# Optimization experiments

Hardware: AMD Instinct MI355X
Metric: run time of the kernel (lower is better)

Reference implementation:

```python
import jax, jax.numpy as jnp
import numpy as np

EPS = 1e-5
SLOPE = 0.2

def _lrelu(x):
    return jnp.where(x >= 0, x, SLOPE * x)

def _bn(x, axes):
    # BatchNorm in training mode with gamma=1, beta=0 (module defaults), biased var
    m = jnp.mean(x, axis=axes, keepdims=True)
    v = jnp.var(x, axis=axes, keepdims=True)
    return (x - m) * jax.lax.rsqrt(v + EPS)

def _knn(x, k):
    # x: [B, C, N] -> idx [B, N, k] of nearest neighbors (incl. self)
    inner = -2.0 * jnp.einsum('bcn,bcm->bnm', x, x)
    xx = jnp.sum(x * x, axis=1)  # [B, N]
    d = -xx[:, :, None] - inner - xx[:, None, :]  # negative squared dist
    return jax.lax.top_k(d, k)[1]

def _graph_feature(x, k):
    # x: [B, C, N] -> [B, 2C, N, k] of (neighbor - center, center)
    idx = _knn(x, k)                       # [B, N, k]
    xt = jnp.transpose(x, (0, 2, 1))       # [B, N, C]
    feat = jax.vmap(lambda xb, ib: xb[ib])(xt, idx)  # [B, N, k, C]
    center = xt[:, :, None, :]
    out = jnp.concatenate([feat - center, jnp.broadcast_to(center, feat.shape)], axis=-1)
    return jnp.transpose(out, (0, 3, 1, 2))

def _conv2(w, x):   # 1x1 conv2d: x [B,C,N,K]
    return jnp.einsum('oc,bcnk->bonk', w, x)

def _conv1(w, x):   # 1x1 conv1d: x [B,C,N]
    return jnp.einsum('oc,bcn->bon', w, x)

def _pool(xyz, feature, wp, bp, kp):
    # dropout is identity in eval mode
    proj = _conv1(wp, feature) + bp[None, :, None]     # [B, C, N]
    vector = jnp.max(proj, axis=-1, keepdims=True)     # [B, C, 1]
    scores = jax.nn.sigmoid(jnp.sum(feature * vector, axis=1))  # [B, N]
    values, idx = jax.lax.top_k(scores, kp)            # [B, kp]
    node_static = jnp.take_along_axis(xyz, idx[:, None, :], axis=2)
    node_feature = jnp.take_along_axis(feature, idx[:, None, :], axis=2)
    v = values[:, None, :]
    return node_static * v, node_feature * v


def setup_inputs() -> dict:
    key = jax.random.key(0)
    ks = jax.random.split(key, 20)
    def rn(i, shape, s=0.05):
        return jax.random.normal(ks[i], shape, dtype=jnp.float32) * s
    return {
        'x': jax.random.normal(ks[0], (16, 3, 2048), dtype=jnp.float32),
        'w1': rn(1, (64, 6)), 'w2': rn(2, (64, 128)), 'w2m': rn(3, (1024, 128)),
        'w3': rn(4, (128, 256)), 'w4': rn(5, (128, 256)), 'w4m': rn(6, (1024, 256)),
        'w5': rn(7, (256, 512)), 'w5m': rn(8, (1024, 256)),
        'wp1': rn(9, (128, 128)), 'bp1': rn(10, (128,)),
        'wp2': rn(11, (256, 256)), 'bp2': rn(12, (256,)),
        'wl1': rn(13, (512, 3072)),
        'wl2': rn(14, (256, 512)), 'bl2': rn(15, (256,)),
        'wl3': rn(16, (40, 256)), 'bl3': rn(17, (40,)),
    }


def reference(x, w1, w2, w2m, w3, w4, w4m, w5, w5m, wp1, bp1, wp2, bp2, wl1, wl2, bl2, wl3, bl3):
    k = 20
    xyz = x
    # stage 1 (N=2048)
    h = _lrelu(_bn(_conv2(w1, _graph_feature(x, k)), (0, 2, 3)))
    x1 = jnp.max(h, axis=-1)                       # [B, 64, N]
    h = _lrelu(_bn(_conv2(w2, _graph_feature(x1, k)), (0, 2, 3)))
    x2 = jnp.max(h, axis=-1)                       # [B, 64, N]
    xt1_ = jnp.concatenate([x1, x2], axis=1)       # [B, 128, N]
    xt1 = _lrelu(_bn(_conv1(w2m, xt1_), (0, 2)))   # [B, 1024, N]
    node1, nf1 = _pool(xyz, xt1_, wp1, bp1, 256)   # [B,3,256], [B,128,256]
    # stage 2 (256 nodes, k//2)
    h = _lrelu(_bn(_conv2(w3, _graph_feature(nf1, k // 2)), (0, 2, 3)))
    x3 = jnp.max(h, axis=-1)                       # [B, 128, 256]
    h = _lrelu(_bn(_conv2(w4, _graph_feature(x3, k // 2)), (0, 2, 3)))
    x4 = jnp.max(h, axis=-1)
    xt2_ = jnp.concatenate([x3, x4], axis=1)       # [B, 256, 256]
    xt2 = _lrelu(_bn(_conv1(w4m, xt2_), (0, 2)))   # [B, 1024, 256]
    node2, nf2 = _pool(node1, xt2_, wp2, bp2, 64)  # [B,3,64], [B,256,64]
    # stage 3 (64 nodes, k//4)
    h = _lrelu(_bn(_conv2(w5, _graph_feature(nf2, k // 4)), (0, 2, 3)))
    x5 = jnp.max(h, axis=-1)                       # [B, 256, 64]
    xt3 = _lrelu(_bn(_conv1(w5m, x5), (0, 2)))     # [B, 1024, 64]
    # global max pools + head (dropout = identity in eval)
    g = jnp.concatenate([jnp.max(xt1, -1), jnp.max(xt2, -1), jnp.max(xt3, -1)], axis=1)  # [B, 3072]
    h = _lrelu(_bn(g @ wl1.T, (0,)))
    h = _lrelu(_bn(h @ wl2.T + bl2, (0,)))
    out = h @ wl3.T + bl3                          # [B, 40]
    return (out, node1, node2)
```

## Files before the change

kernel.cpp:

```cpp
#include <hip/hip_runtime.h>
#include <cmath>
#include <cstdint>
#include <cstddef>

typedef unsigned int u32;
typedef unsigned short u16;
typedef unsigned long long u64;
typedef __attribute__((ext_vector_type(8))) short short8v;
typedef __attribute__((ext_vector_type(4))) float f32x4;

#define TPB 256
#define EPSV 1e-5f
#define SLP 0.2f

__device__ __forceinline__ float lrelu(float x){ return x >= 0.f ? x : SLP*x; }
__device__ __forceinline__ u32 encf(float f){ u32 u=__float_as_uint(f); return (u&0x80000000u)? ~u : (u|0x80000000u); }
__device__ __forceinline__ float decf(u32 e){ return (e&0x80000000u)? __uint_as_float(e&0x7FFFFFFFu) : __uint_as_float(~e); }
__device__ __forceinline__ u16 f2b(float f){ u32 u=__float_as_uint(f); return (u16)((u + 0x7FFFu + ((u>>16)&1u))>>16); }
__device__ __forceinline__ float b2f(u16 h){ return __uint_as_float(((u32)h)<<16); }

__global__ void k_detect(const u16* __restrict__ raw, int n, int* __restrict__ flag){
  __shared__ float red[TPB];
  int tid=threadIdx.x; float m=0.f;
  for(int i=tid;i<n;i+=TPB){
    float v=fabsf(b2f(raw[i]));
    if(!isnan(v) && !isinf(v) && v>m) m=v;
  }
  red[tid]=m; __syncthreads();
  for(int s=TPB/2;s>0;s>>=1){ if(tid<s) red[tid]=fmaxf(red[tid],red[tid+s]); __syncthreads(); }
  if(tid==0) *flag = (red[0] > 1000.f) ? 1 : 0;
}

struct CvtArgs{ const void* s[18]; float* d[18]; int n[18]; };
__global__ void k_cvt_all(CvtArgs a, const int* __restrict__ flag){
  int z=blockIdx.y; int n=a.n[z]; int f=*flag;
  const void* s=a.s[z]; float* d=a.d[z];
  for(int i=blockIdx.x*TPB+threadIdx.x; i<n; i+=gridDim.x*TPB)
    d[i] = f ? ((const float*)s)[i] : b2f(((const u16*)s)[i]);
}

__global__ void k_castw(const float* __restrict__ W, u16* __restrict__ Wb, int n){
  int i=blockIdx.x*TPB+threadIdx.x; if(i<n) Wb[i]=f2b(W[i]);
}

__global__ void k_xpose_bf(const float* __restrict__ X, u16* __restrict__ Xb,
                           int ldC, int C, int N){
  __shared__ float t[32][33];
  int b=blockIdx.z;
  int c0=blockIdx.y*32, n0=blockIdx.x*32;
  int tx=threadIdx.x&31, ty=threadIdx.x>>5;
  const float* Xs = X + (size_t)b*ldC*N;
  #pragma unroll
  for(int i=0;i<4;i++){
    int c=c0+ty+i*8;
    t[ty+i*8][tx] = (c<C && n0+tx<N) ? Xs[(size_t)c*N + n0+tx] : 0.f;
  }
  __syncthreads();
  u16* Ob = Xb + (size_t)b*N*C;
  #pragma unroll
  for(int i=0;i<4;i++){
    int n=n0+ty+i*8;
    if(n<N && c0+tx<C) Ob[(size_t)n*C + c0+tx] = f2b(t[tx][ty+i*8]);
  }
}

template<int KSTEPS>
__global__ __launch_bounds__(256) void k_convmax_mfma(
    const u16* __restrict__ Wb, const u16* __restrict__ Xb,
    u32* __restrict__ gmaxEnc, int gstride, int g_off, double* __restrict__ stats,
    int C, int N, int O){
  int tid=threadIdx.x, lane=tid&63, w=tid>>6;
  int b=blockIdx.z;
  int oW = blockIdx.y*64 + w*16;
  int nB = blockIdx.x*256;
  int row16 = lane&15, grp = lane>>4;
  short8v af[KSTEPS];
  const u16* Wrow = Wb + (size_t)(oW + row16)*C + grp*8;
  #pragma unroll
  for(int ks=0;ks<KSTEPS;ks++) af[ks] = *(const short8v*)(Wrow + ks*32);
  const short8v zb = {0,0,0,0,0,0,0,0};
  f32x4 acc[16];
  #pragma unroll
  for(int t=0;t<16;t++){
    int n = nB + t*16 + row16;
    bool nv = (n < N);
    const u16* Xrow = Xb + ((size_t)b*N + (nv? n:0))*C + grp*8;
    short8v bf[KSTEPS];
    #pragma unroll
    for(int ks=0;ks<KSTEPS;ks++) bf[ks] = nv ? *(const short8v*)(Xrow + ks*32) : zb;
    f32x4 a = {0.f,0.f,0.f,0.f};
    #pragma unroll
    for(int ks=0;ks<KSTEPS;ks++)
      a = __builtin_amdgcn_mfma_f32_16x16x32_bf16(af[ks], bf[ks], a, 0, 0, 0);
    acc[t]=a;
  }
  float mxr[4], s1r[4], s2r[4];
  #pragma unroll
  for(int r=0;r<4;r++){ mxr[r]=-INFINITY; s1r[r]=0.f; s2r[r]=0.f; }
  #pragma unroll
  for(int t=0;t<16;t++){
    int n = nB + t*16 + row16;
    bool nv = (n<N);
    #pragma unroll
    for(int r=0;r<4;r++){
      float y = acc[t][r];
      if(nv){ mxr[r]=fmaxf(mxr[r],y); s1r[r]+=y; s2r[r]+=y*y; }
    }
  }
  #pragma unroll
  for(int s=1;s<16;s<<=1){
    #pragma unroll
    for(int r=0;r<4;r++){
      mxr[r]=fmaxf(mxr[r], __shfl_xor(mxr[r], s));
      s1r[r]+=__shfl_xor(s1r[r], s);
      s2r[r]+=__shfl_xor(s2r[r], s);
    }
  }
  if(row16==0){
    #pragma unroll
    for(int r=0;r<4;r++){
      int o = oW + grp*4 + r;
      atomicMax(&gmaxEnc[(size_t)b*gstride + g_off + o], encf(mxr[r]));
      atomicAdd(&stats[2*o], (double)s1r[r]);
      atomicAdd(&stats[2*o+1], (double)s2r[r]);
    }
  }
}

__global__ void k_sqnorm(const float* __restrict__ X, float* __restrict__ xx, int B, int ldC, int C, int N){
  int i=blockIdx.x*TPB+threadIdx.x; if(i>=B*N) return;
  int b=i/N, n=i-b*N;
  const float* p = X + ((size_t)b*ldC)*N + n;
  float s=0.f;
  for(int c=0;c<C;c++){ float x=p[(size_t)c*N]; s+=x*x; }
  xx[i]=s;
}

template<int JMAX, int CT>
__global__ __launch_bounds__(256) void k_knn_fused(
    const float* __restrict__ X, const float* __restrict__ xx,
    int ldC, int KSEL, int* __restrict__ idxOut){
  const int N = JMAX*64;
  extern __shared__ float sm[];
  __shared__ u64 cand[4][128];
  int tid=threadIdx.x, lane=tid&63, w=tid>>6;
  int b, row0;
  if constexpr (JMAX==32){
    int lin=blockIdx.x, xcd=lin&7, j=lin>>3;
    b = xcd + ((j>>9)<<3);
    row0 = (j&511)*4;
  } else {
    b = blockIdx.y; row0 = blockIdx.x*4;
  }
  const float* Xb = X + (size_t)b*ldC*N;
  const float* xxb = xx + (size_t)b*N;

  if constexpr (JMAX==32){
    int c0 = tid*4;
    float4 acc0[4], acc1[4];
    #pragma unroll
    for(int r=0;r<4;r++){ acc0[r]=make_float4(0,0,0,0); acc1[r]=make_float4(0,0,0,0); }
    #pragma unroll 4
    for(int c=0;c<CT;c++){
      const float* Xc = Xb + (size_t)c*N;
      float4 b0 = *(const float4*)&Xc[c0];
      float4 b1 = *(const float4*)&Xc[c0+1024];
      #pragma unroll
      for(int r=0;r<4;r++){
        float a = Xc[row0+r];
        acc0[r].x += a*b0.x; acc0[r].y += a*b0.y; acc0[r].z += a*b0.z; acc0[r].w += a*b0.w;
        acc1[r].x += a*b1.x; acc1[r].y += a*b1.y; acc1[r].z += a*b1.z; acc1[r].w += a*b1.w;
      }
    }
    float4 xm0 = *(const float4*)&xxb[c0];
    float4 xm1 = *(const float4*)&xxb[c0+1024];
    #pragma unroll
    for(int r=0;r<4;r++){
      float xr = xxb[row0+r];
      float4 d0, d1;
      d0.x=2.f*acc0[r].x-xr-xm0.x; d0.y=2.f*acc0[r].y-xr-xm0.y;
      d0.z=2.f*acc0[r].z-xr-xm0.z; d0.w=2.f*acc0[r].w-xr-xm0.w;
      d1.x=2.f*acc1[r].x-xr-xm1.x; d1.y=2.f*acc1[r].y-xr-xm1.y;
      d1.z=2.f*acc1[r].z-xr-xm1.z; d1.w=2.f*acc1[r].w-xr-xm1.w;
      *(float4*)&sm[r*N + c0]        = d0;
      *(float4*)&sm[r*N + c0 + 1024] = d1;
    }
  } else {
    int tcol = (tid < N)? tid : (tid & (N-1));
    float acc[4];
    #pragma unroll
    for(int r=0;r<4;r++) acc[r]=0.f;
    #pragma unroll 4
    for(int c=0;c<CT;c++){
      const float* Xc = Xb + (size_t)c*N;
      float bv = Xc[tcol];
      #pragma unroll
      for(int r=0;r<4;r++) acc[r] += Xc[row0+r]*bv;
    }
    float xm = xxb[tcol];
    #pragma unroll
    for(int r=0;r<4;r++) sm[r*N + tcol] = 2.f*acc[r] - xxb[row0+r] - xm;
  }
  __syncthreads();

  u64* cw = cand[w];
  int r = w;
  const float* Sr = sm + (size_t)r*N;
  u32 ev[JMAX];
  if constexpr (JMAX>=4){
    #pragma unroll
    for(int ch=0;ch<JMAX/4;ch++){
      float4 v = *(const float4*)&Sr[ch*256 + lane*4];
      ev[ch*4+0]=encf(v.x); ev[ch*4+1]=encf(v.y); ev[ch*4+2]=encf(v.z); ev[ch*4+3]=encf(v.w);
    }
  } else {
    ev[0]=encf(Sr[lane]);
  }
  int* op = idxOut + ((size_t)b*N + row0 + r)*KSEL;
  if constexpr (JMAX>=8){
    u32 vmax=ev[0];
    #pragma unroll
    for(int j=1;j<JMAX;j++) vmax = vmax>ev[j]? vmax:ev[j];
    u32 lo=0u, hi=0xFFFFFFFFu;
    while(lo<hi){
      u32 d=hi-lo; u32 mid=lo+(d>>1)+(d&1u);
      int cnum=(int)__popcll(__ballot(vmax>=mid));
      if(cnum>=KSEL) lo=mid; else hi=mid-1u;
    }
    u32 T=lo;
    u64 lml=((u64)1<<lane)-1ull;
    u32 base=0;
    #pragma unroll
    for(int j=0;j<JMAX;j++){
      bool p = ev[j]>=T;
      u64 mk=__ballot(p);
      u32 pos=base+(u32)__popcll(mk&lml);
      int m = (j>>2)*256 + lane*4 + (j&3);
      if(p && pos<128u) cw[pos] = ((u64)ev[j]<<32) | (u64)(u32)(~(u32)m);
      base += (u32)__popcll(mk);
    }
    int nc=(int)base;
    if(nc<=64){
      u64 cv = cw[lane];
      if(lane>=nc) cv=0ull;
      #pragma unroll
      for(int kk=2;kk<=64;kk<<=1){
        #pragma unroll
        for(int jj=kk>>1;jj>0;jj>>=1){
          u64 p=__shfl_xor(cv,jj);
          bool takeMax=(((lane&jj)!=0)==((lane&kk)==0));
          u64 mx=cv>p?cv:p, mn=cv>p?p:cv;
          cv=takeMax?mx:mn;
        }
      }
      if(lane>=64-KSEL) op[63-lane]=(int)(~(u32)cv);
    } else if(nc<=128){
      u64 c0v=cw[lane], c1v=cw[64+lane];
      if(64+lane>=nc) c1v=0ull;
      u64 kl=~0ull;
      for(int t=0;t<KSEL;t++){
        u64 bk=(c0v<kl)?c0v:0ull;
        if(c1v<kl&&c1v>bk) bk=c1v;
        #pragma unroll
        for(int s=1;s<64;s<<=1){u64 ok=__shfl_xor(bk,s); if(ok>bk)bk=ok;}
        if(lane==0) op[t]=(int)(~(u32)bk);
        kl=bk;
      }
    } else {
      u64 kl=~0ull;
      for(int t=0;t<KSEL;t++){
        u64 bk=0ull;
        #pragma unroll
        for(int j=0;j<JMAX;j++){
          int m = (j>>2)*256 + lane*4 + (j&3);
          u64 kj=((u64)ev[j]<<32)|(u64)(u32)(~(u32)m);
          if(kj<kl&&kj>bk) bk=kj;
        }
        #pragma unroll
        for(int s=1;s<64;s<<=1){u64 ok=__shfl_xor(bk,s); if(ok>bk)bk=ok;}
        if(lane==0) op[t]=(int)(~(u32)bk);
        kl=bk;
      }
    }
  } else {
    u64 key[JMAX];
    #pragma unroll
    for(int j=0;j<JMAX;j++){
      int m = (JMAX>=4)? ((j>>2)*256 + lane*4 + (j&3)) : lane;
      key[j]=((u64)ev[j]<<32)|(u64)(u32)(~(u32)m);
    }
    u64 kl=~0ull;
    for(int t=0;t<KSEL;t++){
      u64 bk=0ull;
      #pragma unroll
      for(int j=0;j<JMAX;j++){ u64 kj=key[j]; if(kj<kl&&kj>bk) bk=kj; }
      #pragma unroll
      for(int s=1;s<64;s<<=1){u64 ok=__shfl_xor(bk,s); if(ok>bk)bk=ok;}
      if(lane==0) op[t]=(int)(~(u32)bk);
      kl=bk;
    }
  }
}

__global__ void k_topk_sort(const float* __restrict__ S, int M, int K,
                            int* __restrict__ idxOut, float* __restrict__ valOut){
  extern __shared__ u64 key[];
  int b=blockIdx.x, tid=threadIdx.x;
  const float* Sr = S + (size_t)b*M;
  for(int i=tid;i<M;i+=TPB)
    key[i] = ((u64)(~encf(Sr[i]))<<32) | (u32)i;
  __syncthreads();
  for(int k=2;k<=M;k<<=1){
    for(int j=k>>1;j>0;j>>=1){
      for(int i=tid;i<M;i+=TPB){
        int ixj=i^j;
        if(ixj>i){
          u64 a=key[i], c=key[ixj];
          bool up=((i&k)==0);
          if(up ? (a>c) : (a<c)){ key[i]=c; key[ixj]=a; }
        }
      }
      __syncthreads();
    }
  }
  for(int p=tid;p<K;p+=TPB){
    u64 kk=key[p];
    idxOut[(size_t)b*K+p]=(int)(u32)(kk&0xFFFFFFFFull);
    valOut[(size_t)b*K+p]=decf(~(u32)(kk>>32));
  }
}

__global__ __launch_bounds__(256) void k_uv_t(
    const float* __restrict__ X, int ldC, const float* __restrict__ W,
    float* __restrict__ U, float* __restrict__ V, int C, int N, int O){
  extern __shared__ float wsm[];
  int tid=threadIdx.x, b=blockIdx.z;
  int o0=blockIdx.y*8;
  for(int i=tid;i<8*C;i+=TPB){
    int o=i/C, c=i-o*C;
    const float* Wr = W + (size_t)(o0+o)*2*C;
    float wa=Wr[c], wb=Wr[C+c];
    wsm[(size_t)(o*C+c)*2  ]=wa;
    wsm[(size_t)(o*C+c)*2+1]=wb-wa;
  }
  __syncthreads();
  int n=blockIdx.x*TPB+tid;
  bool act=(n<N); int nc=act? n:0;
  const float* Xb = X + ((size_t)b*ldC)*N + nc;
  float u[8], v[8];
  #pragma unroll
  for(int o=0;o<8;o++){ u[o]=0.f; v[o]=0.f; }
  for(int c=0;c<C;c++){
    float x = Xb[(size_t)c*N];
    #pragma unroll
    for(int o=0;o<8;o++){
      float2 wv = *(const float2*)&wsm[(size_t)(o*C+c)*2];
      u[o] += wv.x*x;
      v[o] += wv.y*x;
    }
  }
  if(act){
    #pragma unroll
    for(int o=0;o<8;o++){
      size_t off=((size_t)b*O+o0+o)*N+n;
      U[off]=u[o]; V[off]=v[o];
    }
  }
}

template<int KT, int OT>
__global__ void k_nbr_t(const float* __restrict__ U, const float* __restrict__ V, const int* __restrict__ idx,
                        float* __restrict__ outBase, int ldCout, int ch_off,
                        double* __restrict__ stats, int O, int N){
  __shared__ double redS[4][OT], redQ[4][OT];
  int tid=threadIdx.x, lane=tid&63, wv=tid>>6;
  int n = blockIdx.x*TPB+tid;
  int o0 = blockIdx.y*OT, b = blockIdx.z;
  bool act = (n<N);
  int nc = act? n : (N-1);
  int jr[KT];
  const int* jp = idx + ((size_t)b*N+nc)*KT;
  #pragma unroll
  for(int k=0;k<KT;k++){ int j=jp[k]; jr[k] = ((unsigned)j<(unsigned)N)? j : 0; }
  for(int oo=0;oo<OT;oo++){
    const float* Ur = U + ((size_t)b*O+o0+oo)*N;
    float mx=-INFINITY, s1=0.f, s2=0.f;
    #pragma unroll
    for(int k=0;k<KT;k++){ float u=Ur[jr[k]]; mx=fmaxf(mx,u); s1+=u; s2+=u*u; }
    float v = V[((size_t)b*O+o0+oo)*N+nc];
    if(act) outBase[((size_t)b*ldCout+ch_off+o0+oo)*N+n] = mx+v;
    double cs = act ? ((double)s1 + (double)KT*(double)v) : 0.0;
    double cq = act ? ((double)s2 + 2.0*(double)v*(double)s1 + (double)KT*(double)v*(double)v) : 0.0;
    #pragma unroll
    for(int s=1;s<64;s<<=1){ cs += __shfl_xor(cs,s); cq += __shfl_xor(cq,s); }
    if(lane==0){ redS[wv][oo]=cs; redQ[wv][oo]=cq; }
  }
  __syncthreads();
  if(tid<OT){
    double s=0,q=0;
    #pragma unroll
    for(int w=0;w<4;w++){ s+=redS[w][tid]; q+=redQ[w][tid]; }
    atomicAdd(&stats[2*(o0+tid)], s);
    atomicAdd(&stats[2*(o0+tid)+1], q);
  }
}

__global__ void k_bnact(float* __restrict__ out, int ldCout, int ch_off, const double* __restrict__ stats,
                        int O, int N, double cnt){
  int n=blockIdx.x*TPB+threadIdx.x; if(n>=N) return;
  int o=blockIdx.y, b=blockIdx.z;
  double m=stats[2*o]/cnt;
  double var=stats[2*o+1]/cnt - m*m;
  float s=rsqrtf((float)var+EPSV);
  size_t p=((size_t)b*ldCout+ch_off+o)*N+n;
  float h=out[p];
  out[p] = lrelu((float)((double)h-m)*s);
}

template<int PTS>
__global__ void k_convmax(const float* __restrict__ X, int ldC, const float* __restrict__ W, const float* __restrict__ bias,
                          u32* __restrict__ gmaxEnc, int gstride, int g_off, double* __restrict__ stats,
                          int C, int N, int O){
  __shared__ float red[4*16*3];
  int tid=threadIdx.x, ot=blockIdx.y, b=blockIdx.z;
  int lane=tid&63, wv=tid>>6;
  int n0 = blockIdx.x*TPB*PTS + tid*PTS;
  bool act = (n0 < N);
  int n0c = act ? n0 : (N-PTS);
  const float* Xb = X + ((size_t)b*ldC)*N;
  const float* Wr = W + (size_t)ot*16*C;
  float acc[16][PTS];
  #pragma unroll
  for(int oo=0;oo<16;oo++)
    #pragma unroll
    for(int p=0;p<PTS;p++) acc[oo][p]=0.f;
  for(int c=0;c<C;c+=4){
    float xv[4][PTS];
    #pragma unroll
    for(int cc=0;cc<4;cc++){
      if(PTS==4){
        float4 t = *(const float4*)&Xb[(size_t)(c+cc)*N + n0c];
        xv[cc][0]=t.x; xv[cc][1]=t.y; xv[cc][2]=t.z; xv[cc][3]=t.w;
      } else {
        xv[cc][0]=Xb[(size_t)(c+cc)*N + n0c];
      }
    }
    #pragma unroll
    for(int oo=0;oo<16;oo++){
      float w0=Wr[oo*C+c], w1=Wr[oo*C+c+1], w2=Wr[oo*C+c+2], w3=Wr[oo*C+c+3];
      #pragma unroll
      for(int p=0;p<PTS;p++)
        acc[oo][p] += w0*xv[0][p] + w1*xv[1][p] + w2*xv[2][p] + w3*xv[3][p];
    }
  }
  bool hs = (stats!=nullptr);
  #pragma unroll
  for(int oo=0;oo<16;oo++){
    float bval = bias? bias[ot*16+oo] : 0.f;
    float mx=-INFINITY, s1=0.f, s2=0.f;
    #pragma unroll
    for(int p=0;p<PTS;p++){
      float y=acc[oo][p]+bval;
      if(act && n0+p<N){ mx=fmaxf(mx,y); s1+=y; s2+=y*y; }
    }
    #pragma unroll
    for(int s=1;s<64;s<<=1){
      mx=fmaxf(mx,__shfl_xor(mx,s));
      if(hs){ s1+=__shfl_xor(s1,s); s2+=__shfl_xor(s2,s); }
    }
    if(lane==0){ red[(wv*16+oo)*3]=mx; red[(wv*16+oo)*3+1]=s1; red[(wv*16+oo)*3+2]=s2; }
  }
  __syncthreads();
  if(tid<16){
    int oo=tid, o=ot*16+oo;
    float mx=red[oo*3], s1=red[oo*3+1], s2=red[oo*3+2];
    #pragma unroll
    for(int w=1;w<4;w++){ mx=fmaxf(mx,red[(w*16+oo)*3]); s1+=red[(w*16+oo)*3+1]; s2+=red[(w*16+oo)*3+2]; }
    atomicMax(&gmaxEnc[(size_t)b*gstride+g_off+o], encf(mx));
    if(hs){ atomicAdd(&stats[2*o],(double)s1); atomicAdd(&stats[2*o+1],(double)s2); }
  }
}

__global__ void k_gfinal(const u32* __restrict__ gmaxEnc, int gstride, int g_off, const double* __restrict__ stats,
                         float* __restrict__ G, int B, int O, double cnt){
  int i=blockIdx.x*TPB+threadIdx.x; if(i>=B*O) return;
  int b=i/O, o=i-b*O;
  double m=stats[2*o]/cnt;
  double var=stats[2*o+1]/cnt - m*m;
  float s=rsqrtf((float)var+EPSV);
  float x=decf(gmaxEnc[(size_t)b*gstride+g_off+o]);
  G[(size_t)b*gstride+g_off+o]=lrelu((float)((double)x-m)*s);
}

__global__ void k_scores(const float* __restrict__ X, int ldC, const u32* __restrict__ vecEnc,
                         float* __restrict__ sc, int C, int N){
  int n=blockIdx.x*TPB+threadIdx.x; if(n>=N) return;
  int b=blockIdx.y;
  const float* Xb = X + ((size_t)b*ldC)*N + n;
  double s=0;
  for(int c=0;c<C;c++) s += (double)Xb[(size_t)c*N]*(double)decf(vecEnc[(size_t)b*C+c]);
  float sf=(float)s;
  sc[(size_t)b*N+n]=1.f/(1.f+expf(-sf));
}

__global__ void k_pgather(const float* __restrict__ xyz, int ldCx, const float* __restrict__ feat, int ldCf,
                          const int* __restrict__ pidx, const float* __restrict__ pval,
                          float* __restrict__ nodeOut, float* __restrict__ nfOut, int Cf, int Nin, int Kp){
  int b=blockIdx.y;
  int i=blockIdx.x*TPB+threadIdx.x;
  int total=(3+Cf)*Kp; if(i>=total) return;
  int c=i/Kp, p=i-c*Kp;
  int j=pidx[(size_t)b*Kp+p]; if((unsigned)j>=(unsigned)Nin) j=0;
  float v=pval[(size_t)b*Kp+p];
  if(c<3) nodeOut[((size_t)b*3+c)*Kp+p]=xyz[((size_t)b*ldCx+c)*Nin+j]*v;
  else { int cf=c-3; nfOut[((size_t)b*Cf+cf)*Kp+p]=feat[((size_t)b*ldCf+cf)*Nin+j]*v; }
}

__global__ void k_fc_wave(const float* __restrict__ A, const float* __restrict__ W, const float* __restrict__ bias,
                          float* __restrict__ Y, int B, int IN, int OUT){
  int gw = (blockIdx.x*blockDim.x + threadIdx.x) >> 6;
  if(gw >= B*OUT) return;
  int lane = threadIdx.x & 63;
  int b = gw/OUT, j = gw - b*OUT;
  const float4* a4 = (const float4*)(A + (size_t)b*IN);
  const float4* w4 = (const float4*)(W + (size_t)j*IN);
  int n4 = IN >> 2;
  float s = 0.f;
  for(int t=lane; t<n4; t+=64){
    float4 av=a4[t], wv=w4[t];
    s += av.x*wv.x + av.y*wv.y + av.z*wv.z + av.w*wv.w;
  }
  #pragma unroll
  for(int sh=1; sh<64; sh<<=1) s += __shfl_xor(s, sh);
  if(lane==0) Y[gw] = s + (bias? bias[j]:0.f);
}

__global__ void k_bnb(const float* __restrict__ Y, float* __restrict__ H, int B, int F){
  int f=blockIdx.x*TPB+threadIdx.x; if(f>=F) return;
  double s=0,q=0;
  for(int b=0;b<B;b++){ double y=Y[(size_t)b*F+f]; s+=y; q+=y*y; }
  double m=s/B, var=q/B-m*m;
  float sc=rsqrtf((float)var+EPSV);
  for(int b=0;b<B;b++){ float y=Y[(size_t)b*F+f]; H[(size_t)b*F+f]=lrelu((float)((double)y-m)*sc); }
}

__global__ void k_out(const float* __restrict__ OUTF, const float* __restrict__ N1v, const float* __restrict__ N2v,
                      void* __restrict__ dout, const int* __restrict__ flag){
  int i=blockIdx.x*TPB+threadIdx.x; if(i>=16000) return;
  float v = (i<640)? OUTF[i] : (i<12928)? N1v[i-640] : N2v[i-12928];
  if(*flag) ((float*)dout)[i]=v; else ((u16*)dout)[i]=f2b(v);
}

extern "C" void kernel_launch(void* const* d_in, const int* in_sizes, int n_in,
                              void* d_out, int out_size, void* d_ws, size_t ws_size,
                              hipStream_t stream){
  const int B=16;
  char* basep=(char*)d_ws; size_t off=0;
  auto alloc=[&](size_t elems, size_t esz)->void*{
    off=(off+255)&~(size_t)255; void* p=basep+off; off+=elems*esz; return p;
  };
  const int NINP=18;
  const int insz[NINP]={98304,384,8192,131072,32768,32768,262144,131072,262144,16384,128,65536,256,1572864,131072,256,10240,40};
  float* F[NINP];
  for(int i=0;i<NINP;i++) F[i]=(float*)alloc((size_t)insz[i],4);
  float* XF=F[0];
  float *W1F=F[1],*W2F=F[2],*W2MF=F[3],*W3F=F[4],*W4F=F[5],*W4MF=F[6],*W5F=F[7],*W5MF=F[8],
        *WP1F=F[9],*BP1F=F[10],*WP2F=F[11],*BP2F=F[12],*WL1F=F[13],*WL2F=F[14],*BL2F=F[15],*WL3F=F[16],*BL3F=F[17];
  float* XX  =(float*)alloc((size_t)16*2048,4);
  float* U   =(float*)alloc((size_t)16*64*2048,4);
  float* V   =(float*)alloc((size_t)16*64*2048,4);
  float* XT1 =(float*)alloc((size_t)16*128*2048,4);
  float* XT2 =(float*)alloc((size_t)16*256*256,4);
  float* NF1 =(float*)alloc((size_t)16*128*256,4);
  float* NF2 =(float*)alloc((size_t)16*256*64,4);
  float* X5  =(float*)alloc((size_t)16*256*64,4);
  float* NODE1=(float*)alloc((size_t)16*3*256,4);
  float* NODE2=(float*)alloc((size_t)16*3*64,4);
  float* SCORES=(float*)alloc((size_t)16*2048,4);
  float* PVAL1=(float*)alloc((size_t)16*256,4);
  float* PVAL2=(float*)alloc((size_t)16*64,4);
  float* G   =(float*)alloc((size_t)16*3072,4);
  float* Y1  =(float*)alloc((size_t)16*512,4);
  float* H1  =(float*)alloc((size_t)16*512,4);
  float* Y2  =(float*)alloc((size_t)16*256,4);
  float* H2  =(float*)alloc((size_t)16*256,4);
  float* OUTF=(float*)alloc((size_t)16*40,4);
  u32* GMAX  =(u32*)alloc((size_t)16*3072,4);
  u32* VECENC=(u32*)alloc((size_t)16*256,4);
  int* IDX   =(int*)alloc((size_t)16*2048*20,4);
  int* PIDX1 =(int*)alloc((size_t)16*256,4);
  int* PIDX2 =(int*)alloc((size_t)16*64,4);
  double* STATS=(double*)alloc((size_t)2*1024,8);
  int* FLAG  =(int*)alloc(64,4);
  u16* XTB  =(u16*)alloc((size_t)16*2048*128,2);
  u16* WB2M =(u16*)alloc((size_t)131072,2);
  u16* WB4M =(u16*)alloc((size_t)262144,2);
  u16* WB5M =(u16*)alloc((size_t)262144,2);

  k_detect<<<dim3(1),dim3(TPB),0,stream>>>((const u16*)d_in[1], insz[1], FLAG);
  CvtArgs ca;
  for(int i=0;i<NINP;i++){ ca.s[i]=d_in[i]; ca.d[i]=F[i]; ca.n[i]=insz[i]; }
  k_cvt_all<<<dim3(64,NINP),dim3(TPB),0,stream>>>(ca, FLAG);
  k_castw<<<dim3((131072+TPB-1)/TPB),dim3(TPB),0,stream>>>(W2MF,WB2M,131072);
  k_castw<<<dim3((262144+TPB-1)/TPB),dim3(TPB),0,stream>>>(W4MF,WB4M,262144);
  k_castw<<<dim3((262144+TPB-1)/TPB),dim3(TPB),0,stream>>>(W5MF,WB5M,262144);

  auto knn=[&](const float* X, int ldC, int C, int N, int K){
    k_sqnorm<<<dim3((B*N+TPB-1)/TPB),dim3(TPB),0,stream>>>(X,XX,B,ldC,C,N);
    size_t shm=(size_t)4*N*4;
    if(N==2048 && C==3)       k_knn_fused<32,3>  <<<dim3(8192),dim3(256),shm,stream>>>(X,XX,ldC,K,IDX);
    else if(N==2048)          k_knn_fused<32,64> <<<dim3(8192),dim3(256),shm,stream>>>(X,XX,ldC,K,IDX);
    else if(N==256)           k_knn_fused<4,128> <<<dim3(N/4,B),dim3(256),shm,stream>>>(X,XX,ldC,K,IDX);
    else                      k_knn_fused<1,256> <<<dim3(N/4,B),dim3(256),shm,stream>>>(X,XX,ldC,K,IDX);
  };

  auto graph_conv=[&](const float* X, int ldC, int C, int N, int K, const float* W, int O,
                      float* outBase, int ldCout, int ch_off){
    knn(X,ldC,C,N,K);
    size_t wshm=(size_t)8*C*2*4;
    k_uv_t<<<dim3((N+TPB-1)/TPB,O/8,B),dim3(TPB),wshm,stream>>>(X,ldC,W,U,V,C,N,O);
    hipMemsetAsync(STATS,0,2*(size_t)O*sizeof(double),stream);
    dim3 g((N+TPB-1)/TPB, O/8, B);
    if(K==20)      k_nbr_t<20,8><<<g,dim3(TPB),0,stream>>>(U,V,IDX,outBase,ldCout,ch_off,STATS,O,N);
    else if(K==10) k_nbr_t<10,8><<<g,dim3(TPB),0,stream>>>(U,V,IDX,outBase,ldCout,ch_off,STATS,O,N);
    else           k_nbr_t<5,8> <<<g,dim3(TPB),0,stream>>>(U,V,IDX,outBase,ldCout,ch_off,STATS,O,N);
    double cnt=(double)B*(double)N*(double)K;
    k_bnact<<<dim3((N+TPB-1)/TPB,O,B),dim3(TPB),0,stream>>>(outBase,ldCout,ch_off,STATS,O,N,cnt);
  };

  auto convmax_f32=[&](const float* X,int ldC,const float* W,const float* bias,
                   u32* gmax,int gstride,int g_off,double* stats,int C,int N,int O){
    if(N>=1024) k_convmax<4><<<dim3((N+TPB*4-1)/(TPB*4),O/16,B),dim3(TPB),0,stream>>>(X,ldC,W,bias,gmax,gstride,g_off,stats,C,N,O);
    else        k_convmax<1><<<dim3((N+TPB-1)/TPB,O/16,B),dim3(TPB),0,stream>>>(X,ldC,W,bias,gmax,gstride,g_off,stats,C,N,O);
  };

  auto pool=[&](const float* xyzF,int ldCx,const float* featF,int ldCf,int Cf,int Nin,
                const float* WP,const float* BP,int Op,int Kp,
                float* nodeOut,float* nfOut,int* pidx,float* pval){
    hipMemsetAsync(VECENC,0,(size_t)B*Op*4,stream);
    convmax_f32(featF,ldCf,WP,BP,VECENC,Op,0,(double*)nullptr,Cf,Nin,Op);
    k_scores<<<dim3((Nin+TPB-1)/TPB,B),dim3(TPB),0,stream>>>(featF,ldCf,VECENC,SCORES,Cf,Nin);
    k_topk_sort<<<dim3(B),dim3(TPB),(size_t)Nin*8,stream>>>(SCORES,Nin,Kp,pidx,pval);
    k_pgather<<<dim3(((3+Cf)*Kp+TPB-1)/TPB,B),dim3(TPB),0,stream>>>(xyzF,ldCx,featF,ldCf,pidx,pval,nodeOut,nfOut,Cf,Nin,Kp);
  };

  auto gseg=[&](const float* X,int ldC,int C,int N,const u16* WBc,int g_off,double cnt){
    hipMemsetAsync(STATS,0,2*1024*sizeof(double),stream);
    k_xpose_bf<<<dim3((N+31)/32,(C+31)/32,B),dim3(256),0,stream>>>(X,XTB,ldC,C,N);
    dim3 g((N+255)/256, 1024/64, B);
    if(C==128) k_convmax_mfma<4><<<g,dim3(256),0,stream>>>(WBc,XTB,GMAX,3072,g_off,STATS,C,N,1024);
    else       k_convmax_mfma<8><<<g,dim3(256),0,stream>>>(WBc,XTB,GMAX,3072,g_off,STATS,C,N,1024);
    k_gfinal<<<dim3((B*1024+TPB-1)/TPB),dim3(TPB),0,stream>>>(GMAX,3072,g_off,STATS,G,B,1024,cnt);
  };

  graph_conv(XF,3,3,2048,20,W1F,64,XT1,128,0);
  graph_conv(XT1,128,64,2048,20,W2F,64,XT1,128,64);
  hipMemsetAsync(GMAX,0,(size_t)16*3072*4,stream);
  gseg(XT1,128,128,2048,WB2M,0,(double)16*2048);
  pool(XF,3,XT1,128,128,2048,WP1F,BP1F,128,256,NODE1,NF1,PIDX1,PVAL1);
  graph_conv(NF1,128,128,256,10,W3F,128,XT2,256,0);
  graph_conv(XT2,256,128,256,10,W4F,128,XT2,256,128);
  gseg(XT2,256,256,256,WB4M,1024,(double)16*256);
  pool(NODE1,3,XT2,256,256,256,WP2F,BP2F,256,64,NODE2,NF2,PIDX2,PVAL2);
  graph_conv(NF2,256,256,64,5,W5F,256,X5,256,0);
  gseg(X5,256,256,64,WB5M,2048,(double)16*64);
  k_fc_wave<<<dim3((16*512*64+TPB-1)/TPB),dim3(TPB),0,stream>>>(G,WL1F,(const float*)nullptr,Y1,16,3072,512);
  k_bnb<<<dim3((512+TPB-1)/TPB),dim3(TPB),0,stream>>>(Y1,H1,16,512);
  k_fc_wave<<<dim3((16*256*64+TPB-1)/TPB),dim3(TPB),0,stream>>>(H1,WL2F,BL2F,Y2,16,512,256);
  k_bnb<<<dim3((256+TPB-1)/TPB),dim3(TPB),0,stream>>>(Y2,H2,16,256);
  k_fc_wave<<<dim3((16*40*64+TPB-1)/TPB),dim3(TPB),0,stream>>>(H2,WL3F,BL3F,OUTF,16,256,40);
  k_out<<<dim3((16000+TPB-1)/TPB),dim3(TPB),0,stream>>>(OUTF,NODE1,NODE2,(u16*)d_out,FLAG);
}
```

Baseline: 1.137 ms.

## Split N=2048 kNN distance tile into halves to halve shared memory and registers

For the N=2048 kNN kernel, the distance row block is now computed in two 1024-column halves. Each half reuses a 16 KB shared buffer, and its encoded values are read into registers before the next half is written. This halves dynamic shared memory, drops the second accumulator set, and adds a launch-bounds occupancy hint of 6 blocks. The cost is an extra barrier and reading the X rows twice.

```diff
diff --git a/kernel.cpp b/kernel.cpp
--- a/kernel.cpp
+++ b/kernel.cpp
@@ -137,7 +137,7 @@
 }
 
 template<int JMAX, int CT>
-__global__ __launch_bounds__(256) void k_knn_fused(
+__global__ __launch_bounds__(256, 6) void k_knn_fused(
     const float* __restrict__ X, const float* __restrict__ xx,
     int ldC, int KSEL, int* __restrict__ idxOut){
   const int N = JMAX*64;
@@ -155,35 +155,44 @@
   const float* Xb = X + (size_t)b*ldC*N;
   const float* xxb = xx + (size_t)b*N;
 
+  u32 ev[JMAX];
+
   if constexpr (JMAX==32){
     int c0 = tid*4;
-    float4 acc0[4], acc1[4];
-    #pragma unroll
-    for(int r=0;r<4;r++){ acc0[r]=make_float4(0,0,0,0); acc1[r]=make_float4(0,0,0,0); }
-    #pragma unroll 4
-    for(int c=0;c<CT;c++){
-      const float* Xc = Xb + (size_t)c*N;
-      float4 b0 = *(const float4*)&Xc[c0];
-      float4 b1 = *(const float4*)&Xc[c0+1024];
+    #pragma unroll
+    for(int h=0;h<2;h++){
+      float4 acc0[4];
+      #pragma unroll
+      for(int r=0;r<4;r++) acc0[r]=make_float4(0,0,0,0);
+      #pragma unroll 4
+      for(int c=0;c<CT;c++){
+        const float* Xc = Xb + (size_t)c*N;
+        float4 b0 = *(const float4*)&Xc[h*1024 + c0];
+        #pragma unroll
+        for(int r=0;r<4;r++){
+          float a = Xc[row0+r];
+          acc0[r].x += a*b0.x; acc0[r].y += a*b0.y; acc0[r].z += a*b0.z; acc0[r].w += a*b0.w;
+        }
+      }
+      float4 xm0 = *(const float4*)&xxb[h*1024 + c0];
       #pragma unroll
       for(int r=0;r<4;r++){
-        float a = Xc[row0+r];
-        acc0[r].x += a*b0.x; acc0[r].y += a*b0.y; acc0[r].z += a*b0.z; acc0[r].w += a*b0.w;
-        acc1[r].x += a*b1.x; acc1[r].y += a*b1.y; acc1[r].z += a*b1.z; acc1[r].w += a*b1.w;
-      }
-    }
-    float4 xm0 = *(const float4*)&xxb[c0];
-    float4 xm1 = *(const float4*)&xxb[c0+1024];
-    #pragma unroll
-    for(int r=0;r<4;r++){
-      float xr = xxb[row0+r];
-      float4 d0, d1;
-      d0.x=2.f*acc0[r].x-xr-xm0.x; d0.y=2.f*acc0[r].y-xr-xm0.y;
-      d0.z=2.f*acc0[r].z-xr-xm0.z; d0.w=2.f*acc0[r].w-xr-xm0.w;
-      d1.x=2.f*acc1[r].x-xr-xm1.x; d1.y=2.f*acc1[r].y-xr-xm1.y;
-      d1.z=2.f*acc1[r].z-xr-xm1.z; d1.w=2.f*acc1[r].w-xr-xm1.w;
-      *(float4*)&sm[r*N + c0]        = d0;
-      *(float4*)&sm[r*N + c0 + 1024] = d1;
+        float xr = xxb[row0+r];
+        float4 d0;
+        d0.x=2.f*acc0[r].x-xr-xm0.x; d0.y=2.f*acc0[r].y-xr-xm0.y;
+        d0.z=2.f*acc0[r].z-xr-xm0.z; d0.w=2.f*acc0[r].w-xr-xm0.w;
+        *(float4*)&sm[r*1024 + c0] = d0;
+      }
+      __syncthreads();
+      const float* Sr = sm + (size_t)w*1024;
+      #pragma unroll
+      for(int ch=0;ch<4;ch++){
+        float4 v = *(const float4*)&Sr[ch*256 + lane*4];
+        int base = h*16 + ch*4;
+        ev[base+0]=encf(v.x); ev[base+1]=encf(v.y);
+        ev[base+2]=encf(v.z); ev[base+3]=encf(v.w);
+      }
+      if(h==0) __syncthreads();
     }
   } else {
     int tcol = (tid < N)? tid : (tid & (N-1));
@@ -200,23 +209,21 @@
     float xm = xxb[tcol];
     #pragma unroll
     for(int r=0;r<4;r++) sm[r*N + tcol] = 2.f*acc[r] - xxb[row0+r] - xm;
-  }
-  __syncthreads();
+    __syncthreads();
+    const float* Sr = sm + (size_t)w*N;
+    if constexpr (JMAX>=4){
+      #pragma unroll
+      for(int ch=0;ch<JMAX/4;ch++){
+        float4 v = *(const float4*)&Sr[ch*256 + lane*4];
+        ev[ch*4+0]=encf(v.x); ev[ch*4+1]=encf(v.y); ev[ch*4+2]=encf(v.z); ev[ch*4+3]=encf(v.w);
+      }
+    } else {
+      ev[0]=encf(Sr[lane]);
+    }
+  }
 
   u64* cw = cand[w];
-  int r = w;
-  const float* Sr = sm + (size_t)r*N;
-  u32 ev[JMAX];
-  if constexpr (JMAX>=4){
-    #pragma unroll
-    for(int ch=0;ch<JMAX/4;ch++){
-      float4 v = *(const float4*)&Sr[ch*256 + lane*4];
-      ev[ch*4+0]=encf(v.x); ev[ch*4+1]=encf(v.y); ev[ch*4+2]=encf(v.z); ev[ch*4+3]=encf(v.w);
-    }
-  } else {
-    ev[0]=encf(Sr[lane]);
-  }
-  int* op = idxOut + ((size_t)b*N + row0 + r)*KSEL;
+  int* op = idxOut + ((size_t)b*N + row0 + w)*KSEL;
   if constexpr (JMAX>=8){
     u32 vmax=ev[0];
     #pragma unroll
@@ -607,11 +614,10 @@
 
   auto knn=[&](const float* X, int ldC, int C, int N, int K){
     k_sqnorm<<<dim3((B*N+TPB-1)/TPB),dim3(TPB),0,stream>>>(X,XX,B,ldC,C,N);
-    size_t shm=(size_t)4*N*4;
-    if(N==2048 && C==3)       k_knn_fused<32,3>  <<<dim3(8192),dim3(256),shm,stream>>>(X,XX,ldC,K,IDX);
-    else if(N==2048)          k_knn_fused<32,64> <<<dim3(8192),dim3(256),shm,stream>>>(X,XX,ldC,K,IDX);
-    else if(N==256)           k_knn_fused<4,128> <<<dim3(N/4,B),dim3(256),shm,stream>>>(X,XX,ldC,K,IDX);
-    else                      k_knn_fused<1,256> <<<dim3(N/4,B),dim3(256),shm,stream>>>(X,XX,ldC,K,IDX);
+    if(N==2048 && C==3)       k_knn_fused<32,3>  <<<dim3(8192),dim3(256),16384,stream>>>(X,XX,ldC,K,IDX);
+    else if(N==2048)          k_knn_fused<32,64> <<<dim3(8192),dim3(256),16384,stream>>>(X,XX,ldC,K,IDX);
+    else if(N==256)           k_knn_fused<4,128> <<<dim3(N/4,B),dim3(256),(size_t)4*N*4,stream>>>(X,XX,ldC,K,IDX);
+    else                      k_knn_fused<1,256> <<<dim3(N/4,B),dim3(256),(size_t)4*N*4,stream>>>(X,XX,ldC,K,IDX);
   };
 
   auto graph_conv=[&](const float* X, int ldC, int C, int N, int K, const float* W, int O,
```

Result: no change. 1.145 ms (+0.6%).
